# Performance work log

Hardware: AMD Instinct MI355X
Metric: run time of the kernel (lower is better)

The kernel has to match this reference:

```python
import jax, jax.numpy as jnp
import numpy as np

B, T, D, H = 32, 1024, 1024, 1024


def gru_cell(x, h, W_ih, W_hh, b_ih, b_hh):
    # torch.nn.GRUCell math; gate order (r, z, n)
    gi = x @ W_ih.T + b_ih          # [B, 3H]
    gh = h @ W_hh.T + b_hh          # [B, 3H]
    i_r, i_z, i_n = jnp.split(gi, 3, axis=-1)
    h_r, h_z, h_n = jnp.split(gh, 3, axis=-1)
    r = jax.nn.sigmoid(i_r + h_r)
    z = jax.nn.sigmoid(i_z + h_z)
    n = jnp.tanh(i_n + r * h_n)
    return (1.0 - z) * n + z * h


def setup_inputs() -> dict:
    key = jax.random.key(0)
    k = jax.random.split(key, 6)
    scale = np.float32(1.0 / np.sqrt(H))  # torch GRUCell init range
    x = jax.random.normal(k[0], (B, T, D), jnp.float32)
    seg = jax.random.randint(k[1], (B, T), 0, 2).astype(jnp.int32)
    W_ih = jax.random.normal(k[2], (3 * H, D), jnp.float32) * scale
    W_hh = jax.random.normal(k[3], (3 * H, H), jnp.float32) * scale
    b_ih = jax.random.normal(k[4], (3 * H,), jnp.float32) * scale
    b_hh = jax.random.normal(k[5], (3 * H,), jnp.float32) * scale
    return {"x": x, "W_ih": W_ih, "W_hh": W_hh, "b_ih": b_ih, "b_hh": b_hh, "seg": seg}


def reference(x, W_ih, W_hh, b_ih, b_hh, seg):
    # apply_rnn_pack: GRUCell scan with segment-masked reset + ragged pack.
    segf = seg.astype(x.dtype)

    def step(h, inp):
        xt, st = inp                      # xt [B,D], st [B]
        h_new = gru_cell(xt, h, W_ih, W_hh, b_ih, b_hh)
        h_next = st[:, None] * h_new      # reset hidden where seg==0
        return h_next, h_new              # emit pre-reset hidden

    h0 = jnp.zeros((B, H), x.dtype)
    xs = (jnp.swapaxes(x, 0, 1), jnp.swapaxes(segf, 0, 1))
    _, hs = jax.lax.scan(step, h0, xs)    # hs [T,B,H]
    hs = jnp.swapaxes(hs, 0, 1)           # [B,T,H]

    # Pack: write h at step t into slot (#emits before t) iff seg[b,t]==0.
    emit = seg == 0                       # [B,T]
    pos = jnp.cumsum(emit, axis=1) - 1    # destination slot for emitted steps
    pos = jnp.where(emit, pos, T)         # route non-emitted steps to pad slot
    out = jnp.zeros((B, T + 1, H), x.dtype)
    b_idx = jnp.arange(B)[:, None]
    out = out.at[b_idx, pos].set(hs)
    out = out[:, :T]                      # [B,T,H], ragged-padded with zeros
    counts = emit.sum(axis=1)             # per-sample packed lengths (idx)
    return out, counts
```

## Files before the change

kernel.cpp:

```cpp
#include <hip/hip_runtime.h>

#define NB 32
#define NT 1024
#define ND 1024
#define NH 1024
#define G3 3072
#define MROWS 32768
#define HROWS 16512
#define GSROWS 32896
#define TAILG 64

typedef __bf16 bf16x8 __attribute__((ext_vector_type(8)));
typedef float f32x4 __attribute__((ext_vector_type(4)));
typedef unsigned short u16x8 __attribute__((ext_vector_type(8)));
typedef unsigned short u16x4 __attribute__((ext_vector_type(4)));

__device__ __forceinline__ float b2f(unsigned short u){
  union { unsigned int i; float f; } v; v.i = ((unsigned int)u) << 16; return v.f;
}
__device__ __forceinline__ unsigned short f2b(float f){
  union { float f; unsigned int i; } v; v.f = f;
  unsigned int r = (v.i + 0x7FFFu + ((v.i >> 16) & 1u)) >> 16;
  return (unsigned short)r;
}
__device__ __forceinline__ float sigm(float x){ return 1.0f / (1.0f + __expf(-x)); }
__device__ __forceinline__ float tanh_(float x){ return 2.0f / (1.0f + __expf(-2.0f * x)) - 1.0f; }

__device__ __forceinline__ void g2l16(const void* g, void* l){
  __builtin_amdgcn_global_load_lds((__attribute__((address_space(1))) void*)g,
                                   (__attribute__((address_space(3))) void*)l, 16, 0, 0);
}

__device__ __forceinline__ unsigned long long ld_agent_u64(const unsigned short* p){
  return __hip_atomic_load((const unsigned long long*)p, __ATOMIC_RELAXED,
                           __HIP_MEMORY_SCOPE_AGENT);
}
__device__ __forceinline__ unsigned short ld_agent_u16(const unsigned short* p){
  return __hip_atomic_load(p, __ATOMIC_RELAXED, __HIP_MEMORY_SCOPE_AGENT);
}
__device__ __forceinline__ void st_agent_u16(unsigned short* p, unsigned short v){
  __hip_atomic_store(p, v, __ATOMIC_RELAXED, __HIP_MEMORY_SCOPE_AGENT);
}

__global__ __launch_bounds__(256) void k_setup(const float* __restrict__ wih,
    const float* __restrict__ whh, const float* __restrict__ x,
    unsigned short* __restrict__ wih_b, unsigned short* __restrict__ whh_b,
    unsigned short* __restrict__ x_b, int has_xb, f32x4* __restrict__ outv, int out_n4){
  int i0 = blockIdx.x * 256 + threadIdx.x;
  int stride = gridDim.x * 256;
  f32x4 z = {0.f, 0.f, 0.f, 0.f};
  for (int j = i0; j < out_n4; j += stride) __builtin_nontemporal_store(z, &outv[j]);
  int nw4 = (G3 * ND) / 4;
  for (int j = i0; j < nw4; j += stride){
    f32x4 a = ((const f32x4*)wih)[j];
    f32x4 b = ((const f32x4*)whh)[j];
    u16x4 ua = {f2b(a[0]), f2b(a[1]), f2b(a[2]), f2b(a[3])};
    u16x4 ub = {f2b(b[0]), f2b(b[1]), f2b(b[2]), f2b(b[3])};
    ((u16x4*)wih_b)[j] = ua;
    ((u16x4*)whh_b)[j] = ub;
  }
  if (has_xb){
    int nx4 = (MROWS * ND) / 4;
    for (int j = i0; j < nx4; j += stride){
      f32x4 a = ((const f32x4*)x)[j];
      u16x4 u = {f2b(a[0]), f2b(a[1]), f2b(a[2]), f2b(a[3])};
      ((u16x4*)x_b)[j] = u;
    }
  }
}

__global__ __launch_bounds__(1024) void k_segbuild(const int* __restrict__ seg,
    int* __restrict__ ugi, int* __restrict__ uout, int* __restrict__ ulen,
    int* __restrict__ nseg_b,
    int* __restrict__ sgi, int* __restrict__ sout, int* __restrict__ slen,
    int* __restrict__ cnt_ge, int* __restrict__ base_g,
    unsigned int* __restrict__ perm, unsigned int* __restrict__ bar,
    float* __restrict__ counts_out){
  __shared__ int hist[1025];
  __shared__ int sufx[1024];
  __shared__ int pref[1024];
  __shared__ int offs[1025];
  int tid = threadIdx.x;
  int wave = tid >> 6, lane = tid & 63;
  if (tid == 0) *bar = 0u;

  for (int b = wave; b < NB; b += 16){
    int prev = -1;
    int zc = 0;
    for (int c = 0; c < 16; ++c){
      int t = c * 64 + lane;
      int v = seg[b * NT + t];
      unsigned long long mask = __ballot(v == 0);
      unsigned long long below = mask & ((1ULL << lane) - 1ULL);
      if (v == 0){
        int pz = below ? (c * 64 + (63 - __clzll((long long)below))) : prev;
        int eidx = zc + __popcll(below);
        int slot = b * NT + eidx;
        ugi[slot]  = b * NT + (pz + 1);
        uout[slot] = b * NT + eidx;
        ulen[slot] = t - pz;
      }
      if (mask) prev = c * 64 + (63 - __clzll((long long)mask));
      zc += __popcll(mask);
    }
    if (lane == 0){ nseg_b[b] = zc; counts_out[b] = (float)zc; }
  }
  __syncthreads();
  for (int i = tid; i <= 1024; i += 1024) hist[i] = 0;
  __syncthreads();
  for (int s = tid; s < NB * NT; s += 1024){
    int b = s >> 10, j = s & 1023;
    if (j < nseg_b[b]) atomicAdd(&hist[ulen[s]], 1);
  }
  __syncthreads();
  if (tid < 1024) sufx[tid] = hist[tid + 1];
  __syncthreads();
  for (int off = 1; off < 1024; off <<= 1){
    int v = (tid + off < 1024) ? sufx[tid + off] : 0;
    __syncthreads();
    sufx[tid] += v;
    __syncthreads();
  }
  cnt_ge[tid + 1] = sufx[tid];
  if (tid == 0){ cnt_ge[0] = sufx[0]; cnt_ge[1025] = 0; }
  offs[tid] = sufx[tid];
  if (tid == 0) offs[1024] = 0;
  pref[tid] = sufx[tid];
  __syncthreads();
  for (int off = 1; off < 1024; off <<= 1){
    int v = (tid >= off) ? pref[tid - off] : 0;
    __syncthreads();
    pref[tid] += v;
    __syncthreads();
  }
  base_g[tid + 1] = pref[tid];
  if (tid == 0){ base_g[0] = 0; base_g[1025] = pref[1023]; }
  __syncthreads();
  for (int s = tid; s < NB * NT; s += 1024){
    int b = s >> 10, j = s & 1023;
    if (j < nseg_b[b]){
      int len = ulen[s];
      int p = atomicAdd(&offs[len], 1);
      sgi[p] = ugi[s]; sout[p] = uout[s]; slen[p] = len;
    }
  }
  for (int m = tid; m < MROWS; m += 1024) perm[m] = 0xFFFFFFFFu;
  __syncthreads();
  int nseg = cnt_ge[1];
  for (int p = tid; p < nseg; p += 1024){
    int src = sgi[p];
    int len = slen[p];
    perm[src] = (unsigned int)p;
    for (int kk = 1; kk < len; ++kk)
      perm[src + kk] = (unsigned int)(pref[kk - 1] + p);
  }
}

__global__ __launch_bounds__(256, 2) void k_gi_gemm(const float* __restrict__ x,
    const unsigned short* __restrict__ x_b, const unsigned short* __restrict__ wih_b,
    const float* __restrict__ b_ih, const unsigned int* __restrict__ perm,
    unsigned short* __restrict__ gs, int use_xb){
  __shared__ unsigned short Alds[128 * 64];
  __shared__ unsigned short Blds[128 * 64];
  int tid = threadIdx.x;
  int w = tid >> 6, lane = tid & 63;
  int mtile = blockIdx.x / 24, ntile = blockIdx.x % 24;
  int m0 = mtile * 128, n0 = ntile * 128;
  int mh = (w >> 1) * 64, nh = (w & 1) * 64;
  int lrow = lane >> 3;
  int lcol = 8 * ((lane & 7) ^ lrow);
  f32x4 acc[4][4];
#pragma unroll
  for (int i = 0; i < 4; ++i)
#pragma unroll
    for (int j = 0; j < 4; ++j) acc[i][j] = (f32x4){0.f, 0.f, 0.f, 0.f};

  for (int kc = 0; kc < 16; ++kc){
    __syncthreads();
    if (use_xb){
#pragma unroll
      for (int p = 0; p < 4; ++p){
        int s = w * 4 + p;
        g2l16(x_b + (size_t)(m0 + s * 8 + lrow) * ND + kc * 64 + lcol, &Alds[s * 512]);
      }
    } else {
#pragma unroll
      for (int p = 0; p < 4; ++p){
        int e = (p * 256 + tid) * 8;
        int r = e >> 6, c = e & 63;
        const float* src = x + (size_t)(m0 + r) * ND + kc * 64 + c;
        f32x4 f0 = *(const f32x4*)src;
        f32x4 f1 = *(const f32x4*)(src + 4);
        u16x8 u;
        u[0]=f2b(f0[0]); u[1]=f2b(f0[1]); u[2]=f2b(f0[2]); u[3]=f2b(f0[3]);
        u[4]=f2b(f1[0]); u[5]=f2b(f1[1]); u[6]=f2b(f1[2]); u[7]=f2b(f1[3]);
        *(u16x8*)&Alds[r * 64 + (c ^ ((r & 7) << 3))] = u;
      }
    }
#pragma unroll
    for (int p = 0; p < 4; ++p){
      int s = w * 4 + p;
      g2l16(wih_b + (size_t)(n0 + s * 8 + lrow) * ND + kc * 64 + lcol, &Blds[s * 512]);
    }
    __syncthreads();
#pragma unroll
    for (int ks = 0; ks < 2; ++ks){
      int co = ks * 32 + (lane >> 4) * 8;
      int cx = co ^ ((lane & 7) << 3);
      bf16x8 a[4], bb[4];
#pragma unroll
      for (int mi = 0; mi < 4; ++mi)
        a[mi] = *(const bf16x8*)&Alds[(mh + mi * 16 + (lane & 15)) * 64 + cx];
#pragma unroll
      for (int ni = 0; ni < 4; ++ni)
        bb[ni] = *(const bf16x8*)&Blds[(nh + ni * 16 + (lane & 15)) * 64 + cx];
#pragma unroll
      for (int mi = 0; mi < 4; ++mi)
#pragma unroll
        for (int ni = 0; ni < 4; ++ni)
          acc[mi][ni] = __builtin_amdgcn_mfma_f32_16x16x32_bf16(a[mi], bb[ni], acc[mi][ni], 0, 0, 0);
    }
  }
#pragma unroll
  for (int mi = 0; mi < 4; ++mi){
    int rbase = m0 + mh + mi * 16 + (lane >> 4) * 4;
#pragma unroll
    for (int rr = 0; rr < 4; ++rr){
      unsigned int prow = perm[rbase + rr];
      if (prow == 0xFFFFFFFFu) continue;
#pragma unroll
      for (int ni = 0; ni < 4; ++ni){
        int col = n0 + nh + ni * 16 + (lane & 15);
        gs[(size_t)prow * G3 + col] = f2b(acc[mi][ni][rr] + b_ih[col]);
      }
    }
  }
}

__global__ __launch_bounds__(256) void k_step0(const float* __restrict__ b_hh,
    const unsigned short* __restrict__ gs,
    const int* __restrict__ sout, const int* __restrict__ cnt_ge,
    unsigned short* __restrict__ hbuf, float* __restrict__ out){
  int nseg = cnt_ge[1];
  int c2 = cnt_ge[2];
  int total = nseg * 128;
  for (int idx = blockIdx.x * 256 + threadIdx.x; idx < total; idx += gridDim.x * 256){
    int i = idx >> 7;
    int c0 = (idx & 127) * 8;
    bool emit = (i >= c2);
    const unsigned short* g = gs + (size_t)i * G3;
    u16x8 vr = __builtin_nontemporal_load((const u16x8*)(g + c0));
    u16x8 vz = __builtin_nontemporal_load((const u16x8*)(g + NH + c0));
    u16x8 vn = __builtin_nontemporal_load((const u16x8*)(g + 2 * NH + c0));
    float hn[8];
#pragma unroll
    for (int j = 0; j < 8; ++j){
      int c = c0 + j;
      float r = sigm(b2f(vr[j]) + b_hh[c]);
      float z = sigm(b2f(vz[j]) + b_hh[NH + c]);
      float n = tanh_(b2f(vn[j]) + r * b_hh[2 * NH + c]);
      hn[j] = (1.0f - z) * n;
    }
    if (emit){
      float* orow = out + (size_t)sout[i] * NH + c0;
      f32x4 v0 = {hn[0], hn[1], hn[2], hn[3]};
      f32x4 v1 = {hn[4], hn[5], hn[6], hn[7]};
      __builtin_nontemporal_store(v0, (f32x4*)orow);
      __builtin_nontemporal_store(v1, (f32x4*)(orow + 4));
    } else {
      u16x8 u;
#pragma unroll
      for (int j = 0; j < 8; ++j) u[j] = f2b(hn[j]);
      *(u16x8*)(hbuf + (size_t)HROWS * NH + (size_t)i * NH + c0) = u;
    }
  }
}

__device__ __forceinline__ void step_tile(int m0, int nc0, int Ak, int c2, int gbase,
    const unsigned short* __restrict__ whh_b, const float* __restrict__ b_hh,
    const unsigned short* __restrict__ gs, const int* __restrict__ sout,
    const unsigned short* __restrict__ hread, unsigned short* __restrict__ hwrite,
    float* __restrict__ out,
    unsigned short (*Alds)[64 * 128], unsigned short (*Blds)[192 * 128]){
  int tid = threadIdx.x;
  int w = tid >> 6, lane = tid & 63;
  int l15 = lane & 15, l4 = lane >> 4;

#define STAGE2(buf, kc) do {                                                        \
    _Pragma("unroll")                                                               \
    for (int p = 0; p < 4; ++p){                                                    \
      int s = w * 4 + p;                                                            \
      int ar = s * 4 + l4;                                                          \
      int sc = (l15 * 8) ^ ((ar & 7) << 3);                                         \
      g2l16(hread + (size_t)(m0 + ar) * NH + (kc) * 128 + sc, &Alds[buf][s * 512]); \
    }                                                                               \
    _Pragma("unroll")                                                               \
    for (int p = 0; p < 12; ++p){                                                   \
      int s = w * 12 + p;                                                           \
      int br = s * 4 + l4;                                                          \
      int wrow = (br >> 6) * NH + nc0 + (br & 63);                                  \
      int sc = (l15 * 8) ^ ((br & 7) << 3);                                         \
      g2l16(whh_b + (size_t)wrow * NH + (kc) * 128 + sc, &Blds[buf][s * 512]);      \
    }                                                                               \
  } while (0)

  STAGE2(0, 0);

  int c_lane = nc0 + w * 16 + l15;
  float bh_r = b_hh[c_lane], bh_z = b_hh[NH + c_lane], bh_n = b_hh[2 * NH + c_lane];
  unsigned short gr_[4][4], gz_[4][4], gn_[4][4], hv_[4][4];
  int so_[4][4];
#pragma unroll
  for (int a = 0; a < 4; ++a){
#pragma unroll
    for (int rr = 0; rr < 4; ++rr){
      int i = m0 + a * 16 + l4 * 4 + rr;
      const unsigned short* g = gs + (size_t)(gbase + i) * G3 + c_lane;
      gr_[a][rr] = __builtin_nontemporal_load(g);
      gz_[a][rr] = __builtin_nontemporal_load(g + NH);
      gn_[a][rr] = __builtin_nontemporal_load(g + 2 * NH);
      hv_[a][rr] = hread[(size_t)i * NH + c_lane];
      so_[a][rr] = sout[i < MROWS ? i : 0];
    }
  }

  f32x4 acc[4][3];
#pragma unroll
  for (int a = 0; a < 4; ++a)
#pragma unroll
    for (int b = 0; b < 3; ++b) acc[a][b] = (f32x4){0.f, 0.f, 0.f, 0.f};

  __syncthreads();
  int cur = 0;
  for (int kc = 0; kc < 8; ++kc){
    if (kc < 7) STAGE2(cur ^ 1, kc + 1);
#pragma unroll
    for (int ks = 0; ks < 4; ++ks){
      int co = ks * 32 + l4 * 8;
      bf16x8 av[4], bv[3];
#pragma unroll
      for (int a = 0; a < 4; ++a){
        int r = a * 16 + l15;
        av[a] = *(const bf16x8*)&Alds[cur][r * 128 + (co ^ ((r & 7) << 3))];
      }
#pragma unroll
      for (int b = 0; b < 3; ++b){
        int br = 64 * b + w * 16 + l15;
        bv[b] = *(const bf16x8*)&Blds[cur][br * 128 + (co ^ ((br & 7) << 3))];
      }
#pragma unroll
      for (int a = 0; a < 4; ++a)
#pragma unroll
        for (int b = 0; b < 3; ++b)
          acc[a][b] = __builtin_amdgcn_mfma_f32_16x16x32_bf16(av[a], bv[b], acc[a][b], 0, 0, 0);
    }
    __syncthreads();
    cur ^= 1;
  }
#undef STAGE2

#pragma unroll
  for (int a = 0; a < 4; ++a){
#pragma unroll
    for (int rr = 0; rr < 4; ++rr){
      int i = m0 + a * 16 + l4 * 4 + rr;
      if (i >= Ak) continue;
      bool emit = (i >= c2);
      float ghr = acc[a][0][rr] + bh_r;
      float ghz = acc[a][1][rr] + bh_z;
      float ghn = acc[a][2][rr] + bh_n;
      float h = b2f(hv_[a][rr]);
      float r = sigm(b2f(gr_[a][rr]) + ghr);
      float z = sigm(b2f(gz_[a][rr]) + ghz);
      float n = tanh_(b2f(gn_[a][rr]) + r * ghn);
      float hn = (1.0f - z) * n + z * h;
      if (emit) __builtin_nontemporal_store(hn, &out[(size_t)so_[a][rr] * NH + c_lane]);
      else      hwrite[(size_t)i * NH + c_lane] = f2b(hn);
    }
  }
}

__global__ __launch_bounds__(256, 1) void k_step(int k,
    const unsigned short* __restrict__ whh_b, const float* __restrict__ b_hh,
    const unsigned short* __restrict__ gs, const int* __restrict__ base_g,
    const int* __restrict__ sout, const int* __restrict__ cnt_ge,
    unsigned short* __restrict__ hbuf, float* __restrict__ out){
  __shared__ unsigned short Alds[2][64 * 128];
  __shared__ unsigned short Blds[2][192 * 128];
  int Ak = cnt_ge[k + 1];
  if (Ak <= 0) return;
  int c2 = cnt_ge[k + 2];
  int gbase = base_g[k];
  int Mt = (Ak + 63) >> 6;
  int tiles = Mt * 16;
  const unsigned short* hread = hbuf + (size_t)(k & 1) * HROWS * NH;
  unsigned short* hwrite      = hbuf + (size_t)((k + 1) & 1) * HROWS * NH;
  for (int t = blockIdx.x; t < tiles; t += gridDim.x){
    int cs = t & 15, mt = t >> 4;
    step_tile(mt * 64, cs * 64, Ak, c2, gbase, whh_b, b_hh, gs, sout,
              hread, hwrite, out, Alds, Blds);
  }
}

__global__ __launch_bounds__(256, 1) void k_tail(
    const unsigned short* __restrict__ whh_b, const float* __restrict__ b_hh,
    const unsigned short* __restrict__ gs, const int* __restrict__ base_g,
    const int* __restrict__ sout, const int* __restrict__ cnt_ge,
    unsigned short* __restrict__ hbuf, float* __restrict__ out,
    unsigned int* __restrict__ bar){
  __shared__ unsigned short Wlds[48 * 1024];
  int tid = threadIdx.x;
  int w = tid >> 6, lane = tid & 63;
  int l15 = lane & 15, l4 = lane >> 4;
  int cs = blockIdx.x;

#pragma unroll
  for (int p = 0; p < 24; ++p){
    int s = w * 24 + p;
    int r = s >> 1, h = s & 1;
    int grow = (r >> 4) * NH + cs * 16 + (r & 15);
    int cp = h * 512 + lane * 8;
    g2l16(whh_b + (size_t)grow * NH + (cp ^ ((r & 7) << 3)),
          &Wlds[r * 1024 + h * 512 + lane * 8]);
  }
  __syncthreads();

  int c_lane = cs * 16 + l15;
  float bh_r = b_hh[c_lane], bh_z = b_hh[NH + c_lane], bh_n = b_hh[2 * NH + c_lane];

  unsigned int phase = 0;
  for (int k = 5; k <= 1023; ++k){
    int Ak = cnt_ge[k + 1];
    if (Ak <= 0) break;
    int c2 = cnt_ge[k + 2];
    int gbase = base_g[k];
    int Mt16 = (Ak + 15) >> 4;
    const unsigned short* hread = hbuf + (size_t)(k & 1) * HROWS * NH;
    unsigned short* hwrite      = hbuf + (size_t)((k + 1) & 1) * HROWS * NH;

    for (int mt = w; mt < Mt16; mt += 4){
      int m0 = mt * 16;
      unsigned short gr_[4], gz_[4], gn_[4], hv_[4];
      int so_[4];
#pragma unroll
      for (int rr = 0; rr < 4; ++rr){
        int i = m0 + l4 * 4 + rr;
        const unsigned short* g = gs + (size_t)(gbase + i) * G3 + c_lane;
        gr_[rr] = __builtin_nontemporal_load(g);
        gz_[rr] = __builtin_nontemporal_load(g + NH);
        gn_[rr] = __builtin_nontemporal_load(g + 2 * NH);
        hv_[rr] = ld_agent_u16(hread + (size_t)i * NH + c_lane);
        so_[rr] = sout[i < MROWS ? i : 0];
      }

      const unsigned short* arow = hread + (size_t)(m0 + l15) * NH + l4 * 8;
      f32x4 acc0 = {0.f, 0.f, 0.f, 0.f}, acc1 = acc0, acc2 = acc0;
#pragma unroll 8
      for (int ks = 0; ks < 32; ++ks){
        int co = ks * 32 + l4 * 8;
        union { bf16x8 v; unsigned long long q[2]; } a;
        a.q[0] = ld_agent_u64(arow + ks * 32);
        a.q[1] = ld_agent_u64(arow + ks * 32 + 4);
        int cx = co ^ ((l15 & 7) << 3);
        bf16x8 b0 = *(const bf16x8*)&Wlds[(0 * 16 + l15) * 1024 + cx];
        bf16x8 b1 = *(const bf16x8*)&Wlds[(1 * 16 + l15) * 1024 + cx];
        bf16x8 b2 = *(const bf16x8*)&Wlds[(2 * 16 + l15) * 1024 + cx];
        acc0 = __builtin_amdgcn_mfma_f32_16x16x32_bf16(a.v, b0, acc0, 0, 0, 0);
        acc1 = __builtin_amdgcn_mfma_f32_16x16x32_bf16(a.v, b1, acc1, 0, 0, 0);
        acc2 = __builtin_amdgcn_mfma_f32_16x16x32_bf16(a.v, b2, acc2, 0, 0, 0);
      }

#pragma unroll
      for (int rr = 0; rr < 4; ++rr){
        int i = m0 + l4 * 4 + rr;
        if (i >= Ak) continue;
        bool emit = (i >= c2);
        float h = b2f(hv_[rr]);
        float r = sigm(b2f(gr_[rr]) + acc0[rr] + bh_r);
        float z = sigm(b2f(gz_[rr]) + acc1[rr] + bh_z);
        float n = tanh_(b2f(gn_[rr]) + r * (acc2[rr] + bh_n));
        float hn = (1.0f - z) * n + z * h;
        if (emit) __builtin_nontemporal_store(hn, &out[(size_t)so_[rr] * NH + c_lane]);
        else      st_agent_u16(hwrite + (size_t)i * NH + c_lane, f2b(hn));
      }
    }

    ++phase;
    __syncthreads();
    if (threadIdx.x == 0){
      atomicAdd(bar, 1u);
      unsigned int goal = phase * (unsigned int)TAILG;
      while (__hip_atomic_load(bar, __ATOMIC_RELAXED, __HIP_MEMORY_SCOPE_AGENT) < goal)
        __builtin_amdgcn_s_sleep(2);
    }
    __syncthreads();
  }
}

extern "C" void kernel_launch(void* const* d_in, const int* in_sizes, int n_in,
                              void* d_out, int out_size, void* d_ws, size_t ws_size,
                              hipStream_t stream){
  (void)in_sizes; (void)n_in;
  const float* x   = (const float*)d_in[0];
  const float* wih = (const float*)d_in[1];
  const float* whh = (const float*)d_in[2];
  const float* bih = (const float*)d_in[3];
  const float* bhh = (const float*)d_in[4];
  const int*   seg = (const int*)d_in[5];
  float* outp = (float*)d_out;

  char* ws = (char*)d_ws;
  size_t o_wih = 0;
  size_t o_whh = 6291456;
  size_t o_gs  = 12582912;
  size_t o_desc = o_gs + (size_t)GSROWS * G3 * 2;
  size_t o_h    = o_desc + (2u << 20);
  size_t o_xb   = o_h + (size_t)2 * HROWS * NH * 2;
  size_t need_xb = o_xb + (size_t)MROWS * ND * 2;
  int has_xb = (ws_size >= need_xb) ? 1 : 0;

  unsigned short* wih_b = (unsigned short*)(ws + o_wih);
  unsigned short* whh_b = (unsigned short*)(ws + o_whh);
  unsigned short* gsort = (unsigned short*)(ws + o_gs);
  int* ugi  = (int*)(ws + o_desc);
  int* uout = ugi + 32768;
  int* ulen = uout + 32768;
  int* sgi  = ulen + 32768;
  int* sout = sgi + 32768;
  int* slen = sout + 32768;
  int* nsegb = slen + 32768;
  int* cntge = nsegb + 64;
  int* baseg = cntge + 1056;
  unsigned int* perm = (unsigned int*)(baseg + 1056);
  unsigned int* bar  = perm + MROWS;
  unsigned short* hbuf = (unsigned short*)(ws + o_h);
  unsigned short* x_b  = (unsigned short*)(ws + o_xb);

  float* counts_out = outp + (size_t)NB * NT * NH;
  int out_n4 = out_size / 4;

  k_setup<<<dim3(4096), dim3(256), 0, stream>>>(wih, whh, x, wih_b, whh_b, x_b, has_xb,
                                                (f32x4*)d_out, out_n4);

  k_segbuild<<<dim3(1), dim3(1024), 0, stream>>>(seg, ugi, uout, ulen, nsegb,
                                                 sgi, sout, slen, cntge, baseg,
                                                 perm, bar, counts_out);

  k_gi_gemm<<<dim3(256 * 24), dim3(256), 0, stream>>>(x, x_b, wih_b, bih, perm, gsort, has_xb);

  k_step0<<<dim3(1024), dim3(256), 0, stream>>>(bhh, gsort, sout, cntge, hbuf, outp);

  static const int grids[5] = {0, 256, 256, 256, 256};
  for (int k = 1; k <= 4; ++k){
    k_step<<<dim3(grids[k]), dim3(256), 0, stream>>>(k, whh_b, bhh, gsort, baseg,
                                                     sout, cntge, hbuf, outp);
  }

  k_tail<<<dim3(TAILG), dim3(256), 0, stream>>>(whh_b, bhh, gsort, baseg,
                                                sout, cntge, hbuf, outp, bar);
}
```

Measured before the change: 1.007 ms.

## Fuse input-gate GEMM with first-step GRU epilogue using gate-interleaved tiles

Replaces the separate input-projection GEMM and step-0 kernel with one kernel. Each block computes a 64-row tile across the r, z and n gates for 64 hidden columns, so the first timestep's gate nonlinearity can be applied in registers. Rows that belong to step 0 write h or the output directly instead of storing gates to gs and reading them back. It also adds double-buffered LDS staging with K=128 chunks, at the cost of larger shared memory (one block per CU) and a different tile shape.

```diff
diff --git a/kernel.cpp b/kernel.cpp
--- a/kernel.cpp
+++ b/kernel.cpp
@@ -156,122 +156,131 @@
   }
 }
 
-__global__ __launch_bounds__(256, 2) void k_gi_gemm(const float* __restrict__ x,
+__global__ __launch_bounds__(256, 1) void k_gi2(const float* __restrict__ x,
     const unsigned short* __restrict__ x_b, const unsigned short* __restrict__ wih_b,
-    const float* __restrict__ b_ih, const unsigned int* __restrict__ perm,
-    unsigned short* __restrict__ gs, int use_xb){
-  __shared__ unsigned short Alds[128 * 64];
-  __shared__ unsigned short Blds[128 * 64];
+    const float* __restrict__ b_ih, const float* __restrict__ b_hh,
+    const unsigned int* __restrict__ perm, const int* __restrict__ sout,
+    const int* __restrict__ cnt_ge,
+    unsigned short* __restrict__ gs, unsigned short* __restrict__ hbuf,
+    float* __restrict__ out, int use_xb){
+  __shared__ unsigned short Alds[2][64 * 128];
+  __shared__ unsigned short Blds[2][192 * 128];
   int tid = threadIdx.x;
   int w = tid >> 6, lane = tid & 63;
-  int mtile = blockIdx.x / 24, ntile = blockIdx.x % 24;
-  int m0 = mtile * 128, n0 = ntile * 128;
-  int mh = (w >> 1) * 64, nh = (w & 1) * 64;
-  int lrow = lane >> 3;
-  int lcol = 8 * ((lane & 7) ^ lrow);
-  f32x4 acc[4][4];
-#pragma unroll
-  for (int i = 0; i < 4; ++i)
-#pragma unroll
-    for (int j = 0; j < 4; ++j) acc[i][j] = (f32x4){0.f, 0.f, 0.f, 0.f};
-
-  for (int kc = 0; kc < 16; ++kc){
-    __syncthreads();
-    if (use_xb){
-#pragma unroll
-      for (int p = 0; p < 4; ++p){
-        int s = w * 4 + p;
-        g2l16(x_b + (size_t)(m0 + s * 8 + lrow) * ND + kc * 64 + lcol, &Alds[s * 512]);
-      }
-    } else {
-#pragma unroll
-      for (int p = 0; p < 4; ++p){
-        int e = (p * 256 + tid) * 8;
-        int r = e >> 6, c = e & 63;
-        const float* src = x + (size_t)(m0 + r) * ND + kc * 64 + c;
-        f32x4 f0 = *(const f32x4*)src;
-        f32x4 f1 = *(const f32x4*)(src + 4);
-        u16x8 u;
-        u[0]=f2b(f0[0]); u[1]=f2b(f0[1]); u[2]=f2b(f0[2]); u[3]=f2b(f0[3]);
-        u[4]=f2b(f1[0]); u[5]=f2b(f1[1]); u[6]=f2b(f1[2]); u[7]=f2b(f1[3]);
-        *(u16x8*)&Alds[r * 64 + (c ^ ((r & 7) << 3))] = u;
-      }
-    }
-#pragma unroll
-    for (int p = 0; p < 4; ++p){
-      int s = w * 4 + p;
-      g2l16(wih_b + (size_t)(n0 + s * 8 + lrow) * ND + kc * 64 + lcol, &Blds[s * 512]);
-    }
-    __syncthreads();
-#pragma unroll
-    for (int ks = 0; ks < 2; ++ks){
-      int co = ks * 32 + (lane >> 4) * 8;
-      int cx = co ^ ((lane & 7) << 3);
-      bf16x8 a[4], bb[4];
-#pragma unroll
-      for (int mi = 0; mi < 4; ++mi)
-        a[mi] = *(const bf16x8*)&Alds[(mh + mi * 16 + (lane & 15)) * 64 + cx];
-#pragma unroll
-      for (int ni = 0; ni < 4; ++ni)
-        bb[ni] = *(const bf16x8*)&Blds[(nh + ni * 16 + (lane & 15)) * 64 + cx];
-#pragma unroll
-      for (int mi = 0; mi < 4; ++mi)
-#pragma unroll
-        for (int ni = 0; ni < 4; ++ni)
-          acc[mi][ni] = __builtin_amdgcn_mfma_f32_16x16x32_bf16(a[mi], bb[ni], acc[mi][ni], 0, 0, 0);
-    }
-  }
-#pragma unroll
-  for (int mi = 0; mi < 4; ++mi){
-    int rbase = m0 + mh + mi * 16 + (lane >> 4) * 4;
+  int l15 = lane & 15, l4 = lane >> 4;
+  int mtile = blockIdx.x >> 4, cs = blockIdx.x & 15;
+  int m0 = mtile * 64, nc0 = cs * 64;
+  int nseg = cnt_ge[1], c2 = cnt_ge[2];
+
+#define GSTAGE(buf, kc) do {                                                         \
+    if (use_xb){                                                                     \
+      _Pragma("unroll")                                                              \
+      for (int p = 0; p < 4; ++p){                                                   \
+        int s = w * 4 + p;                                                           \
+        int ar = s * 4 + l4;                                                         \
+        int sc = (l15 * 8) ^ ((ar & 7) << 3);                                        \
+        g2l16(x_b + (size_t)(m0 + ar) * ND + (kc) * 128 + sc, &Alds[buf][s * 512]);  \
+      }                                                                              \
+    } else {                                                                         \
+      _Pragma("unroll")                                                              \
+      for (int p = 0; p < 4; ++p){                                                   \
+        int e = (p * 256 + tid) * 8;                                                 \
+        int r = e >> 7, c = e & 127;                                                 \
+        const float* src = x + (size_t)(m0 + r) * ND + (kc) * 128 + c;               \
+        f32x4 f0 = *(const f32x4*)src;                                               \
+        f32x4 f1 = *(const f32x4*)(src + 4);                                         \
+        u16x8 u;                                                                     \
+        u[0]=f2b(f0[0]); u[1]=f2b(f0[1]); u[2]=f2b(f0[2]); u[3]=f2b(f0[3]);          \
+        u[4]=f2b(f1[0]); u[5]=f2b(f1[1]); u[6]=f2b(f1[2]); u[7]=f2b(f1[3]);          \
+        *(u16x8*)&Alds[buf][r * 128 + (c ^ ((r & 7) << 3))] = u;                     \
+      }                                                                              \
+    }                                                                                \
+    _Pragma("unroll")                                                                \
+    for (int p = 0; p < 12; ++p){                                                    \
+      int s = w * 12 + p;                                                            \
+      int br = s * 4 + l4;                                                           \
+      int wrow = (br >> 6) * NH + nc0 + (br & 63);                                   \
+      int sc = (l15 * 8) ^ ((br & 7) << 3);                                          \
+      g2l16(wih_b + (size_t)wrow * NH + (kc) * 128 + sc, &Blds[buf][s * 512]);       \
+    }                                                                                \
+  } while (0)
+
+  GSTAGE(0, 0);
+
+  int c_lane = nc0 + w * 16 + l15;
+  float bi_r = b_ih[c_lane], bi_z = b_ih[NH + c_lane], bi_n = b_ih[2 * NH + c_lane];
+  float bh_r = b_hh[c_lane], bh_z = b_hh[NH + c_lane], bh_n = b_hh[2 * NH + c_lane];
+  unsigned int pr_[4][4];
+  int so_[4][4];
+#pragma unroll
+  for (int a = 0; a < 4; ++a){
 #pragma unroll
     for (int rr = 0; rr < 4; ++rr){
-      unsigned int prow = perm[rbase + rr];
-      if (prow == 0xFFFFFFFFu) continue;
-#pragma unroll
-      for (int ni = 0; ni < 4; ++ni){
-        int col = n0 + nh + ni * 16 + (lane & 15);
-        gs[(size_t)prow * G3 + col] = f2b(acc[mi][ni][rr] + b_ih[col]);
-      }
-    }
-  }
-}
-
-__global__ __launch_bounds__(256) void k_step0(const float* __restrict__ b_hh,
-    const unsigned short* __restrict__ gs,
-    const int* __restrict__ sout, const int* __restrict__ cnt_ge,
-    unsigned short* __restrict__ hbuf, float* __restrict__ out){
-  int nseg = cnt_ge[1];
-  int c2 = cnt_ge[2];
-  int total = nseg * 128;
-  for (int idx = blockIdx.x * 256 + threadIdx.x; idx < total; idx += gridDim.x * 256){
-    int i = idx >> 7;
-    int c0 = (idx & 127) * 8;
-    bool emit = (i >= c2);
-    const unsigned short* g = gs + (size_t)i * G3;
-    u16x8 vr = __builtin_nontemporal_load((const u16x8*)(g + c0));
-    u16x8 vz = __builtin_nontemporal_load((const u16x8*)(g + NH + c0));
-    u16x8 vn = __builtin_nontemporal_load((const u16x8*)(g + 2 * NH + c0));
-    float hn[8];
-#pragma unroll
-    for (int j = 0; j < 8; ++j){
-      int c = c0 + j;
-      float r = sigm(b2f(vr[j]) + b_hh[c]);
-      float z = sigm(b2f(vz[j]) + b_hh[NH + c]);
-      float n = tanh_(b2f(vn[j]) + r * b_hh[2 * NH + c]);
-      hn[j] = (1.0f - z) * n;
-    }
-    if (emit){
-      float* orow = out + (size_t)sout[i] * NH + c0;
-      f32x4 v0 = {hn[0], hn[1], hn[2], hn[3]};
-      f32x4 v1 = {hn[4], hn[5], hn[6], hn[7]};
-      __builtin_nontemporal_store(v0, (f32x4*)orow);
-      __builtin_nontemporal_store(v1, (f32x4*)(orow + 4));
-    } else {
-      u16x8 u;
-#pragma unroll
-      for (int j = 0; j < 8; ++j) u[j] = f2b(hn[j]);
-      *(u16x8*)(hbuf + (size_t)HROWS * NH + (size_t)i * NH + c0) = u;
+      int i = m0 + a * 16 + l4 * 4 + rr;
+      unsigned int pr = perm[i];
+      pr_[a][rr] = pr;
+      so_[a][rr] = (pr < (unsigned int)nseg) ? sout[pr] : 0;
+    }
+  }
+
+  f32x4 acc[4][3];
+#pragma unroll
+  for (int a = 0; a < 4; ++a)
+#pragma unroll
+    for (int b = 0; b < 3; ++b) acc[a][b] = (f32x4){0.f, 0.f, 0.f, 0.f};
+
+  __syncthreads();
+  int cur = 0;
+  for (int kc = 0; kc < 8; ++kc){
+    if (kc < 7) GSTAGE(cur ^ 1, kc + 1);
+#pragma unroll
+    for (int ks = 0; ks < 4; ++ks){
+      int co = ks * 32 + l4 * 8;
+      bf16x8 av[4], bv[3];
+#pragma unroll
+      for (int a = 0; a < 4; ++a){
+        int r = a * 16 + l15;
+        av[a] = *(const bf16x8*)&Alds[cur][r * 128 + (co ^ ((r & 7) << 3))];
+      }
+#pragma unroll
+      for (int b = 0; b < 3; ++b){
+        int br = 64 * b + w * 16 + l15;
+        bv[b] = *(const bf16x8*)&Blds[cur][br * 128 + (co ^ ((br & 7) << 3))];
+      }
+#pragma unroll
+      for (int a = 0; a < 4; ++a)
+#pragma unroll
+        for (int b = 0; b < 3; ++b)
+          acc[a][b] = __builtin_amdgcn_mfma_f32_16x16x32_bf16(av[a], bv[b], acc[a][b], 0, 0, 0);
+    }
+    __syncthreads();
+    cur ^= 1;
+  }
+#undef GSTAGE
+
+  unsigned short* hb1 = hbuf + (size_t)HROWS * NH;
+#pragma unroll
+  for (int a = 0; a < 4; ++a){
+#pragma unroll
+    for (int rr = 0; rr < 4; ++rr){
+      unsigned int pr = pr_[a][rr];
+      if (pr == 0xFFFFFFFFu) continue;
+      float gr = acc[a][0][rr] + bi_r;
+      float gz = acc[a][1][rr] + bi_z;
+      float gn = acc[a][2][rr] + bi_n;
+      if (pr < (unsigned int)nseg){
+        float r = sigm(gr + bh_r);
+        float z = sigm(gz + bh_z);
+        float n = tanh_(gn + r * bh_n);
+        float hn = (1.0f - z) * n;
+        if ((int)pr >= c2) out[(size_t)so_[a][rr] * NH + c_lane] = hn;
+        else               hb1[(size_t)pr * NH + c_lane] = f2b(hn);
+      } else {
+        unsigned short* g = gs + (size_t)pr * G3 + c_lane;
+        g[0]      = f2b(gr);
+        g[NH]     = f2b(gz);
+        g[2 * NH] = f2b(gn);
+      }
     }
   }
 }
@@ -546,9 +555,9 @@
                                                  sgi, sout, slen, cntge, baseg,
                                                  perm, bar, counts_out);
 
-  k_gi_gemm<<<dim3(256 * 24), dim3(256), 0, stream>>>(x, x_b, wih_b, bih, perm, gsort, has_xb);
-
-  k_step0<<<dim3(1024), dim3(256), 0, stream>>>(bhh, gsort, sout, cntge, hbuf, outp);
+  k_gi2<<<dim3((MROWS / 64) * 16), dim3(256), 0, stream>>>(x, x_b, wih_b, bih, bhh,
+                                                           perm, sout, cntge,
+                                                           gsort, hbuf, outp, has_xb);
 
   static const int grids[5] = {0, 256, 256, 256, 256};
   for (int k = 1; k <= 4; ++k){
```

Result: slower. 1.289 ms (+27.9%).
